# Kernel tuning notes

Measured on AMD Instinct MI355X. Metric: run time of the kernel, lower is better.

The kernel has to match this reference:

```python
import jax, jax.numpy as jnp
import numpy as np

SEQ = 4096
DIM = 1024
HEADS = 16
HEAD_DIM = DIM // HEADS


def setup_inputs() -> dict:
    key = jax.random.key(0)
    ks = jax.random.split(key, 11)
    s = 1.0 / np.sqrt(DIM)
    return {
        "cos_freq": jax.random.normal(ks[0], (SEQ, DIM), jnp.float32),
        "sin_freq": jax.random.normal(ks[1], (SEQ, DIM), jnp.float32),
        "inputs": jax.random.normal(ks[2], (SEQ, DIM), jnp.float32),
        "input_mask": jnp.ones((SEQ,), jnp.int32),
        "Wq": jax.random.normal(ks[3], (DIM, DIM), jnp.float32) * s,
        "bq": jax.random.normal(ks[4], (DIM,), jnp.float32) * 0.02,
        "Wk": jax.random.normal(ks[5], (DIM, DIM), jnp.float32) * s,
        "bk": jax.random.normal(ks[6], (DIM,), jnp.float32) * 0.02,
        "Wv": jax.random.normal(ks[7], (DIM, DIM), jnp.float32) * s,
        "bv": jax.random.normal(ks[8], (DIM,), jnp.float32) * 0.02,
        "Wo": jax.random.normal(ks[9], (DIM, DIM), jnp.float32) * s,
        "bo": jax.random.normal(ks[10], (DIM,), jnp.float32) * 0.02,
    }


def _rope(x, cos, sin):
    # rotate-half RoPE applied on the full feature dim before QKV projection
    half = x.shape[-1] // 2
    rot = jnp.concatenate([-x[..., half:], x[..., :half]], axis=-1)
    return x * cos + rot * sin


def reference(cos_freq, sin_freq, inputs, input_mask, Wq, bq, Wk, bk, Wv, bv, Wo, bo):
    S, D = inputs.shape
    H, hd = HEADS, D // HEADS

    # RoPE on query inputs and (self) kv context
    q_in = _rope(inputs, cos_freq, sin_freq)
    kv_in = _rope(inputs, cos_freq, sin_freq)

    # projections (eqx Linear: y = W @ x + b), split heads
    q = (q_in @ Wq.T + bq).reshape(S, H, hd)
    k = (kv_in @ Wk.T + bk).reshape(S, H, hd)
    v = (kv_in @ Wv.T + bv).reshape(S, H, hd)

    # scaled dot-product attention with outer-product mask
    logits = jnp.einsum("qhd,khd->hqk", q / jnp.sqrt(jnp.float32(hd)), k)
    mask = (input_mask[:, None] * input_mask[None, :]) != 0  # [S, S]
    logits = jnp.where(mask[None, :, :], logits, jnp.finfo(logits.dtype).min)
    weights = jax.nn.softmax(logits, axis=-1)  # [H, S, S]

    attn = jnp.einsum("hqk,khd->qhd", weights, v).reshape(S, D)
    out = attn @ Wo.T + bo
    return out + inputs  # residual
```

## Files before the change

### kernel.cpp

```cpp
#include <hip/hip_runtime.h>
#include <hip/hip_bf16.h>


#define SEQ 4096
#define DIM 1024
#define NH 16
#define HD 64

typedef unsigned short u16;
typedef __attribute__((ext_vector_type(4))) u16 u16x4;
typedef __attribute__((ext_vector_type(8))) short s16x8;
typedef __attribute__((ext_vector_type(4))) float f32x4;
typedef __attribute__((ext_vector_type(16))) float f32x16;
typedef __attribute__((ext_vector_type(4))) unsigned u32x4;

static __device__ __forceinline__ u16 f2bf(float f) {
  unsigned u = __builtin_bit_cast(unsigned, f);
  u += 0x7FFF + ((u >> 16) & 1);
  return (u16)(u >> 16);
}

static __device__ __forceinline__ void glds16(const u16* g, u16* l) {
  __builtin_amdgcn_global_load_lds((const __attribute__((address_space(1))) unsigned*)g,
                                   (__attribute__((address_space(3))) unsigned*)l, 16, 0, 0);
}

static __device__ __forceinline__ float fast_exp2(float x) {
#if __has_builtin(__builtin_amdgcn_exp2f)
  return __builtin_amdgcn_exp2f(x);
#else
  return exp2f(x);
#endif
}

static __device__ __forceinline__ unsigned pack_bf(float p0, float p1) {
  return __builtin_amdgcn_perm(__builtin_bit_cast(unsigned, p1),
                               __builtin_bit_cast(unsigned, p0), 0x07060302u);
}

__global__ __launch_bounds__(256) void prep(const float* __restrict__ x,
                                            const float* __restrict__ cs,
                                            const float* __restrict__ sn,
                                            const float* __restrict__ Wq,
                                            const float* __restrict__ Wk,
                                            const float* __restrict__ Wv,
                                            const float* __restrict__ Wo,
                                            u16* __restrict__ Xr,
                                            u16* __restrict__ Wb) {
  int b = blockIdx.x;
  if (b < 4096) {
    int idx = (b * 256 + threadIdx.x) * 4;
    int d = idx & (DIM - 1);
    f32x4 xv = *(const f32x4*)&x[idx];
    f32x4 cv = *(const f32x4*)&cs[idx];
    f32x4 sv = *(const f32x4*)&sn[idx];
    f32x4 rv;
    if (d < DIM / 2) rv = -*(const f32x4*)&x[idx + DIM / 2];
    else             rv =  *(const f32x4*)&x[idx - DIM / 2];
    f32x4 o = xv * cv + rv * sv;
    u16x4 ov;
    for (int i = 0; i < 4; i++) ov[i] = f2bf(o[i]);
    *(u16x4*)&Xr[idx] = ov;
  } else {
    int idx = ((b - 4096) * 256 + threadIdx.x) * 4;
    const int M = 1 << 20;
    const float* src = (idx < M) ? Wq : (idx < 2 * M) ? Wk : (idx < 3 * M) ? Wv : Wo;
    int off = idx & (M - 1);
    f32x4 v = *(const f32x4*)&src[off];
    u16x4 ov;
    for (int i = 0; i < 4; i++) ov[i] = f2bf(v[i]);
    *(u16x4*)&Wb[idx] = ov;
  }
}

__global__ __launch_bounds__(256) void qkv_gemm(const u16* __restrict__ Xr,
                                                const u16* __restrict__ Wb,
                                                const float* __restrict__ bq,
                                                const float* __restrict__ bk,
                                                const float* __restrict__ bv,
                                                u16* __restrict__ Qo,
                                                u16* __restrict__ Ko,
                                                u16* __restrict__ Vt) {
  const int z = blockIdx.z;
  const u16* W = Wb + (size_t)z * DIM * DIM;
  const float* bias = (z == 0) ? bq : (z == 1) ? bk : bv;
  const float scale = (z == 0) ? 0.180336884f : 1.0f;

  const int m0 = blockIdx.x * 128, n0 = blockIdx.y * 128;
  const int tid = threadIdx.x;
  const int w = tid >> 6, lane = tid & 63, quad = lane >> 4, ln = lane & 15;
  const int rowoff = (w >> 1) * 64, coloff = (w & 1) * 64;

  __shared__ __align__(16) u16 SMEM[2][2][128 * 32];
  u16 (*As)[128 * 32] = SMEM[0];
  u16 (*Bs)[128 * 32] = SMEM[1];

  f32x4 acc[4][4];
  for (int i = 0; i < 4; i++)
    for (int j = 0; j < 4; j++) acc[i][j] = (f32x4){0.f, 0.f, 0.f, 0.f};

  for (int t = 0; t < 2; t++) {
    int i = tid + t * 256, r = i >> 2, p = i & 3, cc = (p ^ (r & 3)) * 8;
    glds16(&Xr[(size_t)(m0 + r) * DIM + cc], As[0] + i * 8);
    glds16(&W[(size_t)(n0 + r) * DIM + cc], Bs[0] + i * 8);
  }

  for (int kt = 0; kt < 32; kt++) {
    __syncthreads();
    if (kt < 31) {
      int k0 = (kt + 1) * 32, nb = (kt + 1) & 1;
      for (int t = 0; t < 2; t++) {
        int i = tid + t * 256, r = i >> 2, p = i & 3, cc = (p ^ (r & 3)) * 8;
        glds16(&Xr[(size_t)(m0 + r) * DIM + k0 + cc], As[nb] + i * 8);
        glds16(&W[(size_t)(n0 + r) * DIM + k0 + cc], Bs[nb] + i * 8);
      }
    }
    int bb = kt & 1;
    s16x8 af[4], bf[4];
    for (int i = 0; i < 4; i++)
      af[i] = *(const s16x8*)&As[bb][(rowoff + i * 16 + ln) * 32 + ((quad ^ (ln & 3)) * 8)];
    for (int j = 0; j < 4; j++)
      bf[j] = *(const s16x8*)&Bs[bb][(coloff + j * 16 + ln) * 32 + ((quad ^ (ln & 3)) * 8)];
    for (int i = 0; i < 4; i++)
      for (int j = 0; j < 4; j++)
        acc[i][j] = __builtin_amdgcn_mfma_f32_16x16x32_bf16(af[i], bf[j], acc[i][j], 0, 0, 0);
  }

  if (z < 2) {
    u16* out = (z == 0) ? Qo : Ko;
    for (int i = 0; i < 4; i++)
      for (int j = 0; j < 4; j++)
        for (int r = 0; r < 4; r++) {
          int row = m0 + rowoff + i * 16 + quad * 4 + r;
          int col = n0 + coloff + j * 16 + ln;
          out[(size_t)row * DIM + col] = f2bf((acc[i][j][r] + bias[col]) * scale);
        }
  } else {
    u16* scratch = &SMEM[0][0][0];
    __syncthreads();
    for (int i = 0; i < 4; i++)
      for (int j = 0; j < 4; j++) {
        int rl0 = rowoff + i * 16 + quad * 4;
        int cl = coloff + j * 16 + ln;
        u16x4 pk;
        for (int r = 0; r < 4; r++) pk[r] = f2bf(acc[i][j][r] + bias[n0 + cl]);
        *(u16x4*)&scratch[cl * 128 + (rl0 ^ ((cl & 15) * 8))] = pk;
      }
    __syncthreads();
    int chunk = tid & 15, colg = tid >> 4;
    for (int p = 0; p < 8; p++) {
      int cl = p * 16 + colg;
      s16x8 v = *(const s16x8*)&scratch[cl * 128 + ((chunk * 8) ^ ((cl & 15) * 8))];
      *(s16x8*)&Vt[(size_t)(n0 + cl) * SEQ + m0 + chunk * 8] = v;
    }
  }
}

__global__ __launch_bounds__(256, 2) void attn_kernel(const u16* __restrict__ Q,
                                                      const u16* __restrict__ K,
                                                      const u16* __restrict__ Vt,
                                                      u16* __restrict__ attn) {
  const int b = blockIdx.x;
  const int h = (b & 7) * 2 + ((b >> 3) & 1);
  const int q0 = (b >> 4) * 128;
  const int tid = threadIdx.x;
  const int w = tid >> 6, lane = tid & 63;
  const int l31 = lane & 31, hi = lane >> 5;
  const int e3 = l31 & 7;

  __shared__ __align__(16) u16 Ks[2][2][64 * 64];
  __shared__ __align__(16) u16 Vts[2][2][64 * 64];

  u16* QP = &Ks[1][0][0];
  for (int t = 0; t < 4; t++) {
    int i = tid + t * 256, r = i >> 3, p = i & 7, cc = (p ^ (r & 7)) * 8;
    glds16(&Q[(size_t)(q0 + r) * DIM + h * HD + cc], QP + i * 8);
  }
  const int sr = tid >> 3, pos = tid & 7;
  const int cc = (pos ^ (sr & 7)) * 8;
  const u16* Kg0 = &K[(size_t)sr * DIM + h * HD + cc];
  const u16* Kg1 = &K[(size_t)(sr + 32) * DIM + h * HD + cc];
  const u16* Vg0 = &Vt[(size_t)(h * HD + sr) * SEQ + cc];
  const u16* Vg1 = &Vt[(size_t)(h * HD + sr + 32) * SEQ + cc];

  for (int t = 0; t < 2; t++) {
    glds16(Kg0 + (size_t)t * 64 * DIM, Ks[0][t] + tid * 8);
    glds16(Kg1 + (size_t)t * 64 * DIM, Ks[0][t] + (tid + 256) * 8);
    glds16(Vg0 + t * 64, Vts[0][t] + tid * 8);
    glds16(Vg1 + t * 64, Vts[0][t] + (tid + 256) * 8);
  }
  __syncthreads();

  s16x8 qf[4];
  {
    int qrow = w * 32 + l31;
#pragma unroll
    for (int s = 0; s < 4; s++)
      qf[s] = *(const s16x8*)&QP[qrow * 64 + (((s * 2 + hi) ^ (qrow & 7)) * 8)];
  }

  f32x16 o[2];
#pragma unroll
  for (int db = 0; db < 2; db++)
#pragma unroll
    for (int i = 0; i < 16; i++) o[db][i] = 0.f;
  float lsum = 0.f;
  const float EC = -23.0831206542f;

  for (int rnd = 0; rnd < 32; rnd++) {
    __syncthreads();
    if (rnd < 31) {
      int nb = (rnd + 1) & 1;
      size_t kt = (size_t)(rnd + 1) * 2;
#pragma unroll
      for (int t = 0; t < 2; t++) {
        glds16(Kg0 + (kt + t) * 64 * DIM, Ks[nb][t] + tid * 8);
        glds16(Kg1 + (kt + t) * 64 * DIM, Ks[nb][t] + (tid + 256) * 8);
        glds16(Vg0 + (kt + t) * 64, Vts[nb][t] + tid * 8);
        glds16(Vg1 + (kt + t) * 64, Vts[nb][t] + (tid + 256) * 8);
      }
    }
    const int bb = rnd & 1;
#pragma unroll
    for (int slot = 0; slot < 2; slot++) {
      const u16* Kt = Ks[bb][slot];
      const u16* Vv = Vts[bb][slot];

      f32x16 St[2];
#pragma unroll
      for (int kb = 0; kb < 2; kb++)
#pragma unroll
        for (int i = 0; i < 16; i++) St[kb][i] = EC;
      __builtin_amdgcn_s_setprio(1);
#pragma unroll
      for (int s = 0; s < 4; s++)
#pragma unroll
        for (int kb = 0; kb < 2; kb++) {
          int row = kb * 32 + l31;
          s16x8 kf = *(const s16x8*)&Kt[row * 64 + (((s * 2 + hi) ^ e3) * 8)];
          St[kb] = __builtin_amdgcn_mfma_f32_32x32x16_bf16(kf, qf[s], St[kb], 0, 0, 0);
        }
      __builtin_amdgcn_s_setprio(0);

      s16x8 PA[4];
#pragma unroll
      for (int hf = 0; hf < 4; hf++) {
        int kb = hf >> 1, s0 = (hf & 1) * 8;
        float p[8];
#pragma unroll
        for (int m = 0; m < 8; m++) {
          p[m] = fast_exp2(St[kb][s0 + m]);
          lsum += p[m];
        }
        unsigned A = pack_bf(p[0], p[1]);
        unsigned B = pack_bf(p[4], p[5]);
        unsigned C = pack_bf(p[2], p[3]);
        unsigned D = pack_bf(p[6], p[7]);
        asm volatile("v_permlane32_swap_b32 %0, %1" : "+v"(A), "+v"(B));
        asm volatile("v_permlane32_swap_b32 %0, %1" : "+v"(C), "+v"(D));
        u32x4 wd = {A, C, B, D};
        PA[hf] = __builtin_bit_cast(s16x8, wd);
      }

      __builtin_amdgcn_s_setprio(1);
#pragma unroll
      for (int s = 0; s < 4; s++)
#pragma unroll
        for (int db = 0; db < 2; db++) {
          int row = db * 32 + l31;
          s16x8 vf = *(const s16x8*)&Vv[row * 64 + (((s * 2 + hi) ^ e3) * 8)];
          o[db] = __builtin_amdgcn_mfma_f32_32x32x16_bf16(PA[s], vf, o[db], 0, 0, 0);
        }
      __builtin_amdgcn_s_setprio(0);
    }
  }

  lsum += __shfl_xor(lsum, 32, 64);
  float inv = __builtin_amdgcn_rcpf(lsum);
#pragma unroll
  for (int r = 0; r < 16; r++) {
    int qr = (r & 3) + 8 * (r >> 2) + 4 * hi;
    float iv = __shfl(inv, qr, 64);
    int row = q0 + w * 32 + qr;
#pragma unroll
    for (int db = 0; db < 2; db++)
      attn[(size_t)row * DIM + h * HD + db * 32 + l31] = f2bf(o[db][r] * iv);
  }
}

__global__ __launch_bounds__(256) void out_gemm(const u16* __restrict__ A,
                                                const u16* __restrict__ W,
                                                const float* __restrict__ bo,
                                                const float* __restrict__ resid,
                                                float* __restrict__ out) {
  const int m0 = blockIdx.x * 64, n0 = blockIdx.y * 128;
  const int tid = threadIdx.x;
  const int w = tid >> 6, lane = tid & 63, quad = lane >> 4, ln = lane & 15;
  const int rowoff = (w >> 1) * 32, coloff = (w & 1) * 64;

  __shared__ __align__(16) u16 As[2][64 * 32];
  __shared__ __align__(16) u16 Bs[2][128 * 32];

  f32x4 acc[2][4];
  for (int i = 0; i < 2; i++)
    for (int j = 0; j < 4; j++) acc[i][j] = (f32x4){0.f, 0.f, 0.f, 0.f};

  {
    int i = tid, r = i >> 2, p = i & 3, cc = (p ^ (r & 3)) * 8;
    glds16(&A[(size_t)(m0 + r) * DIM + cc], As[0] + i * 8);
    for (int t = 0; t < 2; t++) {
      int ib = tid + t * 256, rb = ib >> 2, pb = ib & 3, ccb = (pb ^ (rb & 3)) * 8;
      glds16(&W[(size_t)(n0 + rb) * DIM + ccb], Bs[0] + ib * 8);
    }
  }

  for (int kt = 0; kt < 32; kt++) {
    __syncthreads();
    if (kt < 31) {
      int k0 = (kt + 1) * 32, nb = (kt + 1) & 1;
      int i = tid, r = i >> 2, p = i & 3, cc = (p ^ (r & 3)) * 8;
      glds16(&A[(size_t)(m0 + r) * DIM + k0 + cc], As[nb] + i * 8);
      for (int t = 0; t < 2; t++) {
        int ib = tid + t * 256, rb = ib >> 2, pb = ib & 3, ccb = (pb ^ (rb & 3)) * 8;
        glds16(&W[(size_t)(n0 + rb) * DIM + k0 + ccb], Bs[nb] + ib * 8);
      }
    }
    int bb = kt & 1;
    s16x8 af[2], bf[4];
    for (int i = 0; i < 2; i++)
      af[i] = *(const s16x8*)&As[bb][(rowoff + i * 16 + ln) * 32 + ((quad ^ (ln & 3)) * 8)];
    for (int j = 0; j < 4; j++)
      bf[j] = *(const s16x8*)&Bs[bb][(coloff + j * 16 + ln) * 32 + ((quad ^ (ln & 3)) * 8)];
    for (int i = 0; i < 2; i++)
      for (int j = 0; j < 4; j++)
        acc[i][j] = __builtin_amdgcn_mfma_f32_16x16x32_bf16(af[i], bf[j], acc[i][j], 0, 0, 0);
  }

  for (int i = 0; i < 2; i++)
    for (int j = 0; j < 4; j++)
      for (int r = 0; r < 4; r++) {
        int row = m0 + rowoff + i * 16 + quad * 4 + r;
        int col = n0 + coloff + j * 16 + ln;
        out[(size_t)row * DIM + col] = acc[i][j][r] + bo[col] + resid[(size_t)row * DIM + col];
      }
}

extern "C" void kernel_launch(void* const* d_in, const int* in_sizes, int n_in,
                              void* d_out, int out_size, void* d_ws, size_t ws_size,
                              hipStream_t stream) {
  const float* cs = (const float*)d_in[0];
  const float* sn = (const float*)d_in[1];
  const float* x  = (const float*)d_in[2];
  const float* Wq = (const float*)d_in[4];  const float* bq = (const float*)d_in[5];
  const float* Wk = (const float*)d_in[6];  const float* bk = (const float*)d_in[7];
  const float* Wv = (const float*)d_in[8];  const float* bv = (const float*)d_in[9];
  const float* Wo = (const float*)d_in[10]; const float* bo = (const float*)d_in[11];
  float* out = (float*)d_out;

  char* ws = (char*)d_ws;
  u16* Xr = (u16*)(ws + (size_t)0);
  u16* Wb = (u16*)(ws + ((size_t)8 << 20));
  u16* Qb = (u16*)(ws + ((size_t)16 << 20));
  u16* Kb = (u16*)(ws + ((size_t)24 << 20));
  u16* Vt = (u16*)(ws + ((size_t)32 << 20));
  u16* Ab = (u16*)(ws + ((size_t)40 << 20));

  prep<<<8192, 256, 0, stream>>>(x, cs, sn, Wq, Wk, Wv, Wo, Xr, Wb);
  qkv_gemm<<<dim3(32, 8, 3), 256, 0, stream>>>(Xr, Wb, bq, bk, bv, Qb, Kb, Vt);
  attn_kernel<<<512, 256, 0, stream>>>(Qb, Kb, Vt, Ab);
  out_gemm<<<dim3(64, 8), 256, 0, stream>>>(Ab, Wb + ((size_t)3 << 20), bo, x, out);
}
```

Before: 253.4 us.

## Fuse Q/K/V projections into one block sharing the activation tile

The QKV GEMM used to launch a separate grid slice for each of Q, K and V. Each 256-thread block loaded its own copy of the activation tile. Now a single 512-thread block computes all three outputs for a 128x128 tile, loading the activation tile once and three weight tiles into shared memory per k-step. This cuts redundant global reads of X and reduces the block count from 768 to 256. The cost is more LDS per block (64KB), more accumulator registers per thread, and fewer blocks to fill the compute units.

```diff
diff --git a/kernel.cpp b/kernel.cpp
--- a/kernel.cpp
+++ b/kernel.cpp
@@ -73,7 +73,7 @@
   }
 }
 
-__global__ __launch_bounds__(256) void qkv_gemm(const u16* __restrict__ Xr,
+__global__ __launch_bounds__(512) void qkv_gemm(const u16* __restrict__ Xr,
                                                 const u16* __restrict__ Wb,
                                                 const float* __restrict__ bq,
                                                 const float* __restrict__ bk,
@@ -81,79 +81,78 @@
                                                 u16* __restrict__ Qo,
                                                 u16* __restrict__ Ko,
                                                 u16* __restrict__ Vt) {
-  const int z = blockIdx.z;
-  const u16* W = Wb + (size_t)z * DIM * DIM;
-  const float* bias = (z == 0) ? bq : (z == 1) ? bk : bv;
-  const float scale = (z == 0) ? 0.180336884f : 1.0f;
-
   const int m0 = blockIdx.x * 128, n0 = blockIdx.y * 128;
   const int tid = threadIdx.x;
   const int w = tid >> 6, lane = tid & 63, quad = lane >> 4, ln = lane & 15;
-  const int rowoff = (w >> 1) * 64, coloff = (w & 1) * 64;
-
-  __shared__ __align__(16) u16 SMEM[2][2][128 * 32];
-  u16 (*As)[128 * 32] = SMEM[0];
-  u16 (*Bs)[128 * 32] = SMEM[1];
-
-  f32x4 acc[4][4];
-  for (int i = 0; i < 4; i++)
-    for (int j = 0; j < 4; j++) acc[i][j] = (f32x4){0.f, 0.f, 0.f, 0.f};
-
-  for (int t = 0; t < 2; t++) {
-    int i = tid + t * 256, r = i >> 2, p = i & 3, cc = (p ^ (r & 3)) * 8;
-    glds16(&Xr[(size_t)(m0 + r) * DIM + cc], As[0] + i * 8);
-    glds16(&W[(size_t)(n0 + r) * DIM + cc], Bs[0] + i * 8);
-  }
+  const int wr = w >> 1, wc = w & 1;
+
+  __shared__ __align__(16) u16 SMEM[8 * 4096];
+#define AS(buf) (&SMEM[(buf) * 4096])
+#define BS(z, buf) (&SMEM[8192 + ((z) * 2 + (buf)) * 4096])
+
+  f32x4 acc[3][2][4];
+  for (int z = 0; z < 3; z++)
+    for (int i = 0; i < 2; i++)
+      for (int j = 0; j < 4; j++) acc[z][i][j] = (f32x4){0.f, 0.f, 0.f, 0.f};
+
+  const int sr_ = tid >> 2, sp = tid & 3;
+  const int scc = (sp ^ (sr_ & 3)) * 8;
+#define STAGE(k0, buf)                                                                    \
+  {                                                                                       \
+    glds16(&Xr[(size_t)(m0 + sr_) * DIM + (k0) + scc], AS(buf) + tid * 8);                \
+    _Pragma("unroll") for (int z = 0; z < 3; z++)                                         \
+      glds16(&Wb[(size_t)z * DIM * DIM + (size_t)(n0 + sr_) * DIM + (k0) + scc],          \
+             BS(z, buf) + tid * 8);                                                       \
+  }
+
+  STAGE(0, 0);
 
   for (int kt = 0; kt < 32; kt++) {
     __syncthreads();
-    if (kt < 31) {
-      int k0 = (kt + 1) * 32, nb = (kt + 1) & 1;
-      for (int t = 0; t < 2; t++) {
-        int i = tid + t * 256, r = i >> 2, p = i & 3, cc = (p ^ (r & 3)) * 8;
-        glds16(&Xr[(size_t)(m0 + r) * DIM + k0 + cc], As[nb] + i * 8);
-        glds16(&W[(size_t)(n0 + r) * DIM + k0 + cc], Bs[nb] + i * 8);
-      }
-    }
+    if (kt < 31) STAGE((kt + 1) * 32, (kt + 1) & 1);
     int bb = kt & 1;
-    s16x8 af[4], bf[4];
-    for (int i = 0; i < 4; i++)
-      af[i] = *(const s16x8*)&As[bb][(rowoff + i * 16 + ln) * 32 + ((quad ^ (ln & 3)) * 8)];
+    s16x8 af[2], bf[3][4];
+    for (int i = 0; i < 2; i++)
+      af[i] = *(const s16x8*)&AS(bb)[(wr * 32 + i * 16 + ln) * 32 + ((quad ^ (ln & 3)) * 8)];
+    for (int z = 0; z < 3; z++)
+      for (int j = 0; j < 4; j++)
+        bf[z][j] = *(const s16x8*)&BS(z, bb)[(wc * 64 + j * 16 + ln) * 32 + ((quad ^ (ln & 3)) * 8)];
+    for (int z = 0; z < 3; z++)
+      for (int i = 0; i < 2; i++)
+        for (int j = 0; j < 4; j++)
+          acc[z][i][j] = __builtin_amdgcn_mfma_f32_16x16x32_bf16(af[i], bf[z][j], acc[z][i][j], 0, 0, 0);
+  }
+#undef STAGE
+
+  const float scale = 0.180336884f;
+  for (int i = 0; i < 2; i++)
     for (int j = 0; j < 4; j++)
-      bf[j] = *(const s16x8*)&Bs[bb][(coloff + j * 16 + ln) * 32 + ((quad ^ (ln & 3)) * 8)];
-    for (int i = 0; i < 4; i++)
-      for (int j = 0; j < 4; j++)
-        acc[i][j] = __builtin_amdgcn_mfma_f32_16x16x32_bf16(af[i], bf[j], acc[i][j], 0, 0, 0);
-  }
-
-  if (z < 2) {
-    u16* out = (z == 0) ? Qo : Ko;
-    for (int i = 0; i < 4; i++)
-      for (int j = 0; j < 4; j++)
-        for (int r = 0; r < 4; r++) {
-          int row = m0 + rowoff + i * 16 + quad * 4 + r;
-          int col = n0 + coloff + j * 16 + ln;
-          out[(size_t)row * DIM + col] = f2bf((acc[i][j][r] + bias[col]) * scale);
-        }
-  } else {
-    u16* scratch = &SMEM[0][0][0];
-    __syncthreads();
-    for (int i = 0; i < 4; i++)
-      for (int j = 0; j < 4; j++) {
-        int rl0 = rowoff + i * 16 + quad * 4;
-        int cl = coloff + j * 16 + ln;
-        u16x4 pk;
-        for (int r = 0; r < 4; r++) pk[r] = f2bf(acc[i][j][r] + bias[n0 + cl]);
-        *(u16x4*)&scratch[cl * 128 + (rl0 ^ ((cl & 15) * 8))] = pk;
-      }
-    __syncthreads();
-    int chunk = tid & 15, colg = tid >> 4;
-    for (int p = 0; p < 8; p++) {
-      int cl = p * 16 + colg;
-      s16x8 v = *(const s16x8*)&scratch[cl * 128 + ((chunk * 8) ^ ((cl & 15) * 8))];
-      *(s16x8*)&Vt[(size_t)(n0 + cl) * SEQ + m0 + chunk * 8] = v;
-    }
-  }
+      for (int r = 0; r < 4; r++) {
+        int row = m0 + wr * 32 + i * 16 + quad * 4 + r;
+        int col = n0 + wc * 64 + j * 16 + ln;
+        Qo[(size_t)row * DIM + col] = f2bf((acc[0][i][j][r] + bq[col]) * scale);
+        Ko[(size_t)row * DIM + col] = f2bf(acc[1][i][j][r] + bk[col]);
+      }
+
+  u16* scratch = &SMEM[0];
+  __syncthreads();
+  for (int i = 0; i < 2; i++)
+    for (int j = 0; j < 4; j++) {
+      int rl0 = wr * 32 + i * 16 + quad * 4;
+      int cl = wc * 64 + j * 16 + ln;
+      u16x4 pk;
+      for (int r = 0; r < 4; r++) pk[r] = f2bf(acc[2][i][j][r] + bv[n0 + cl]);
+      *(u16x4*)&scratch[cl * 128 + (rl0 ^ ((cl & 15) * 8))] = pk;
+    }
+  __syncthreads();
+  for (int p = 0; p < 4; p++) {
+    int tt = tid + p * 512;
+    int cl = tt >> 4, chunk = tt & 15;
+    s16x8 v = *(const s16x8*)&scratch[cl * 128 + ((chunk * 8) ^ ((cl & 15) * 8))];
+    *(s16x8*)&Vt[(size_t)(n0 + cl) * SEQ + m0 + chunk * 8] = v;
+  }
+#undef AS
+#undef BS
 }
 
 __global__ __launch_bounds__(256, 2) void attn_kernel(const u16* __restrict__ Q,
@@ -366,7 +365,7 @@
   u16* Ab = (u16*)(ws + ((size_t)40 << 20));
 
   prep<<<8192, 256, 0, stream>>>(x, cs, sn, Wq, Wk, Wv, Wo, Xr, Wb);
-  qkv_gemm<<<dim3(32, 8, 3), 256, 0, stream>>>(Xr, Wb, bq, bk, bv, Qb, Kb, Vt);
+  qkv_gemm<<<dim3(32, 8), 512, 0, stream>>>(Xr, Wb, bq, bk, bv, Qb, Kb, Vt);
   attn_kernel<<<512, 256, 0, stream>>>(Qb, Kb, Vt, Ab);
   out_gemm<<<dim3(64, 8), 256, 0, stream>>>(Ab, Wb + ((size_t)3 << 20), bo, x, out);
 }
```

New measurement: 246.5 us. 2.7% less time.
